# Optimization experiments

Hardware: AMD Instinct MI355X
Metric: run time of the kernel (lower is better)

## Reference

```python
import jax, jax.numpy as jnp
import numpy as np

N_HEAD = 4
EPS = 1e-5

def _layernorm(x, g, b):
    mu = jnp.mean(x, axis=-1, keepdims=True)
    var = jnp.mean(jnp.square(x - mu), axis=-1, keepdims=True)
    return (x - mu) * jax.lax.rsqrt(var + EPS) * g + b

def setup_inputs() -> dict:
    key = jax.random.key(0)
    ks = jax.random.split(key, 16)
    B, T, F = 8, 1024, 256
    dk = F // N_HEAD
    s = 1.0 / np.sqrt(F)
    return {
        "x": jax.random.normal(ks[0], (B, T, F), jnp.float32),
        "q_in": jax.random.normal(ks[1], (B, T, F), jnp.float32),
        "pos_k": jax.random.normal(ks[2], (T, T, dk), jnp.float32),
        "mask": jax.random.randint(ks[3], (B, T, T), 0, 2, jnp.int32),
        "ln_g": jnp.ones((F,), jnp.float32),
        "ln_b": jnp.zeros((F,), jnp.float32),
        "Wq": jax.random.normal(ks[4], (F, F), jnp.float32) * s,
        "bq": jnp.zeros((F,), jnp.float32),
        "Wk": jax.random.normal(ks[5], (F, F), jnp.float32) * s,
        "bk": jnp.zeros((F,), jnp.float32),
        "Wv": jax.random.normal(ks[6], (F, F), jnp.float32) * s,
        "bv": jnp.zeros((F,), jnp.float32),
        "Wo": jax.random.normal(ks[7], (F, F), jnp.float32) * s,
        "bo": jnp.zeros((F,), jnp.float32),
    }

def reference(x, q_in, pos_k, mask, ln_g, ln_b, Wq, bq, Wk, bk, Wv, bv, Wo, bo):
    B, T2, F = x.shape
    T1 = q_in.shape[1]
    h = N_HEAD
    dk = F // h
    xn = _layernorm(x, ln_g, ln_b)
    # (B, T, h, dk) -> (B, h, T, dk)
    q = (q_in @ Wq + bq).reshape(B, T1, h, dk).transpose(0, 2, 1, 3)
    k = (xn @ Wk + bk).reshape(B, T2, h, dk).transpose(0, 2, 1, 3)
    v = (xn @ Wv + bv).reshape(B, T2, h, dk).transpose(0, 2, 1, 3)
    A = jnp.einsum('bhqd,bhkd->bhqk', q, k)
    # relative position bias: B[b,h,q,t] = sum_d q[b,h,q,d] * pos_k[q,t,d]
    Bmat = jnp.einsum('bhqd,qtd->bhqt', q, pos_k)
    scores = (A + Bmat) / np.sqrt(dk)
    m = (mask[:, None, :, :] == 0)  # (B,1,T1,T2)
    min_val = jnp.finfo(scores.dtype).min
    scores = jnp.where(m, min_val, scores)
    attn = jax.nn.softmax(scores, axis=-1)
    attn = jnp.where(m, 0.0, attn)
    out = jnp.einsum('bhqk,bhkd->bhqd', attn, v)
    out = out.transpose(0, 2, 1, 3).reshape(B, T1, F)
    return out @ Wo + bo
```

## Files before the change

### kernel.cpp

```cpp
#include <hip/hip_runtime.h>
#include <hip/hip_bf16.h>

#define TT 1024
#define FF 256

typedef float  f4v  __attribute__((ext_vector_type(4)));
typedef float  f16v __attribute__((ext_vector_type(16)));
typedef __bf16 bf8v __attribute__((ext_vector_type(8)));
typedef unsigned short us8v __attribute__((ext_vector_type(8)));
typedef unsigned short us4v __attribute__((ext_vector_type(4)));

static __device__ __forceinline__ unsigned short f2bf(float x) {
    return __builtin_bit_cast(unsigned short, (__bf16)x);
}
static __device__ __forceinline__ float bf2f(unsigned short u) {
    return (float)__builtin_bit_cast(__bf16, u);
}
static __device__ __forceinline__ bf8v us2bf(us8v v) {
    return __builtin_bit_cast(bf8v, v);
}

__global__ __launch_bounds__(256) void k_wprep(
    const float* __restrict__ Wq, const float* __restrict__ Wk,
    const float* __restrict__ Wv, const float* __restrict__ Wo,
    unsigned short* __restrict__ Wt)
{
    __shared__ unsigned short T[32][36];
    const float* W = (blockIdx.y == 0) ? Wq : (blockIdx.y == 1) ? Wk
                   : (blockIdx.y == 2) ? Wv : Wo;
    unsigned short* dst = Wt + (blockIdx.y << 16);
    const int kt = (blockIdx.x >> 3) << 5, nt = (blockIdx.x & 7) << 5;
    const int r = threadIdx.x >> 3, c0 = (threadIdx.x & 7) << 2;
    const f4v w = *(const f4v*)&W[(kt + r) * FF + nt + c0];
    #pragma unroll
    for (int j = 0; j < 4; ++j) T[c0 + j][r] = f2bf(w[j]);
    __syncthreads();
    *(us4v*)&dst[(nt + r) * FF + kt + c0] = *(const us4v*)&T[r][c0];
}

__global__ __launch_bounds__(256) void k_ln(
    const float* __restrict__ x, const float* __restrict__ qin,
    const float* __restrict__ lng, const float* __restrict__ lnb,
    unsigned short* __restrict__ xn_bf, unsigned short* __restrict__ qin_bf)
{
    const int tid = threadIdx.x, lane = tid & 63, wv = tid >> 6;
    const int r0 = blockIdx.x << 4;

    #pragma unroll
    for (int u = 0; u < 4; ++u) {
        const int i4 = ((u << 8) + tid) << 2;
        const int r = i4 >> 8, c = i4 & 255;
        const f4v qv = *(const f4v*)&qin[(r0 + r) * FF + c];
        us4v o;
        #pragma unroll
        for (int j = 0; j < 4; ++j) o[j] = f2bf(qv[j]);
        *(us4v*)&qin_bf[(r0 + r) * FF + c] = o;
    }

    #pragma unroll
    for (int rr = 0; rr < 4; ++rr) {
        const int row = r0 + (wv << 2) + rr;
        float v[4], s = 0.f, s2 = 0.f;
        #pragma unroll
        for (int c4 = 0; c4 < 4; ++c4) {
            v[c4] = x[row * FF + (c4 << 6) + lane];
            s += v[c4]; s2 += v[c4] * v[c4];
        }
        #pragma unroll
        for (int off = 1; off < 64; off <<= 1) {
            s  += __shfl_xor(s, off);
            s2 += __shfl_xor(s2, off);
        }
        const float mu  = s * (1.f / FF);
        const float rsd = rsqrtf(s2 * (1.f / FF) - mu * mu + 1e-5f);
        #pragma unroll
        for (int c4 = 0; c4 < 4; ++c4) {
            const int c = (c4 << 6) + lane;
            xn_bf[row * FF + c] = f2bf((v[c4] - mu) * rsd * lng[c] + lnb[c]);
        }
    }
}

__global__ __launch_bounds__(256) void k_proj(
    const unsigned short* __restrict__ qin_bf, const unsigned short* __restrict__ xn_bf,
    const unsigned short* __restrict__ Wt,
    const float* __restrict__ bq, const float* __restrict__ bk, const float* __restrict__ bv,
    unsigned short* __restrict__ Qh, unsigned short* __restrict__ Kh,
    unsigned short* __restrict__ Vt)
{
    __shared__ __align__(16) unsigned short As[64 * 264];
    const int z = blockIdx.y;
    const unsigned short* A = (z == 0) ? qin_bf : xn_bf;
    const unsigned short* W = Wt + (z << 16);
    const float* bias = (z == 0) ? bq : (z == 1) ? bk : bv;
    unsigned short* dst = (z == 0) ? Qh : (z == 1) ? Kh : Vt;
    const int tid = threadIdx.x;
    const int m0 = blockIdx.x << 6;

    #pragma unroll
    for (int u = 0; u < 8; ++u) {
        const int idx = (u << 8) + tid;
        const int r = idx >> 5, c = (idx & 31) << 3;
        *(us8v*)&As[r * 264 + c] = *(const us8v*)&A[(m0 + r) * FF + c];
    }
    __syncthreads();

    const int lane = tid & 63, nw = tid >> 6, gq = lane >> 5, l31 = lane & 31;
    f16v acc[2][2];
    #pragma unroll
    for (int i = 0; i < 2; ++i)
        #pragma unroll
        for (int j = 0; j < 2; ++j)
            #pragma unroll
            for (int e = 0; e < 16; ++e) acc[i][j][e] = 0.f;

    for (int ks = 0; ks < 16; ++ks) {
        const int k0 = (ks << 4) + (gq << 3);
        bf8v af[2], wf[2];
        af[0] = us2bf(*(const us8v*)&As[l31 * 264 + k0]);
        af[1] = us2bf(*(const us8v*)&As[(32 + l31) * 264 + k0]);
        wf[0] = us2bf(*(const us8v*)&W[((nw << 6) + l31) * FF + k0]);
        wf[1] = us2bf(*(const us8v*)&W[((nw << 6) + 32 + l31) * FF + k0]);
        if (z == 2) {
            #pragma unroll
            for (int ti = 0; ti < 2; ++ti)
                #pragma unroll
                for (int tj = 0; tj < 2; ++tj)
                    acc[ti][tj] = __builtin_amdgcn_mfma_f32_32x32x16_bf16(
                        wf[tj], af[ti], acc[ti][tj], 0, 0, 0);
        } else {
            #pragma unroll
            for (int ti = 0; ti < 2; ++ti)
                #pragma unroll
                for (int tj = 0; tj < 2; ++tj)
                    acc[ti][tj] = __builtin_amdgcn_mfma_f32_32x32x16_bf16(
                        af[ti], wf[tj], acc[ti][tj], 0, 0, 0);
        }
    }

    if (z != 2) {
        #pragma unroll
        for (int ti = 0; ti < 2; ++ti)
            #pragma unroll
            for (int tj = 0; tj < 2; ++tj)
                #pragma unroll
                for (int reg = 0; reg < 16; ++reg) {
                    const int row = (reg & 3) + ((reg >> 2) << 3) + (gq << 2);
                    const int tg = m0 + (ti << 5) + row;
                    const int n = (nw << 6) + (tj << 5) + l31;
                    float val = acc[ti][tj][reg] + bias[n];
                    if (z == 0) val *= 0.125f;
                    const int b = tg >> 10, t = tg & 1023;
                    dst[(((b << 2) + nw) << 16) + (t << 6) + (tj << 5) + l31] = f2bf(val);
                }
    } else {
        #pragma unroll
        for (int ti = 0; ti < 2; ++ti)
            #pragma unroll
            for (int tj = 0; tj < 2; ++tj)
                #pragma unroll
                for (int reg = 0; reg < 16; ++reg) {
                    const int row = (reg & 3) + ((reg >> 2) << 3) + (gq << 2);
                    const int d = (tj << 5) + row;
                    const int tg = m0 + (ti << 5) + l31;
                    const float val = acc[ti][tj][reg] + bias[(nw << 6) + d];
                    const int b = tg >> 10, t = tg & 1023;
                    dst[(((b << 2) + nw) << 16) + (d << 10) + t] = f2bf(val);
                }
    }
}

__global__ __launch_bounds__(256) void k_bterm(
    const unsigned short* __restrict__ Qh, const float* __restrict__ posk,
    const int* __restrict__ mask, unsigned short* __restrict__ Bm)
{
    const int tid = threadIdx.x, lane = tid & 63, wv = tid >> 6;
    const int gq = lane >> 5, m = lane & 31;
    const int q = blockIdx.y;
    const int t = (blockIdx.x << 7) + (wv << 5) + m;

    bf8v afr[4];
    #pragma unroll
    for (int kk = 0; kk < 4; ++kk)
        afr[kk] = us2bf(*(const us8v*)&Qh[(m << 16) + (q << 6) + (kk << 4) + (gq << 3)]);

    bf8v bfr[4];
    #pragma unroll
    for (int kk = 0; kk < 4; ++kk) {
        const int d0 = (kk << 4) + (gq << 3);
        const f4v p0 = *(const f4v*)&posk[(((q << 10) + t) << 6) + d0];
        const f4v p1 = *(const f4v*)&posk[(((q << 10) + t) << 6) + d0 + 4];
        bf8v bb;
        bb[0] = (__bf16)p0[0]; bb[1] = (__bf16)p0[1];
        bb[2] = (__bf16)p0[2]; bb[3] = (__bf16)p0[3];
        bb[4] = (__bf16)p1[0]; bb[5] = (__bf16)p1[1];
        bb[6] = (__bf16)p1[2]; bb[7] = (__bf16)p1[3];
        bfr[kk] = bb;
    }

    f16v acc;
    #pragma unroll
    for (int i = 0; i < 16; ++i) acc[i] = 0.f;
    #pragma unroll
    for (int kk = 0; kk < 4; ++kk)
        acc = __builtin_amdgcn_mfma_f32_32x32x16_bf16(afr[kk], bfr[kk], acc, 0, 0, 0);

    int mk[4];
    #pragma unroll
    for (int g = 0; g < 4; ++g)
        mk[g] = mask[(((g << 1) + gq) << 20) + (q << 10) + t];
    #pragma unroll
    for (int reg = 0; reg < 16; ++reg) {
        const int g = reg >> 2;
        const int bhr = (reg & 3) + (g << 3) + (gq << 2);
        const float val = mk[g] ? acc[reg] : -3.0e38f;
        Bm[(bhr << 20) + (q << 10) + t] = f2bf(val);
    }
}

__global__ __launch_bounds__(256, 4) void k_attn(
    const unsigned short* __restrict__ Qh, const unsigned short* __restrict__ Kh,
    const unsigned short* __restrict__ Vt, const unsigned short* __restrict__ Bm,
    unsigned short* __restrict__ aout_bf)
{
    __shared__ __align__(16) unsigned short PsT[4][16 * 132];
    __shared__ __align__(16) float OLDS[2][16 * 68];
    __shared__ float MLDS[2][2][16];

    const int tid = threadIdx.x, lane = tid & 63, wv = tid >> 6;
    const int l15 = lane & 15, quad = lane >> 4;
    const int qg = wv & 1, th = wv >> 1;
    const int blk = blockIdx.x;
    const int bh = ((blk & 7) << 2) | ((blk >> 3) & 3);
    const int qt = blk >> 5;
    const int b = bh >> 2, h = bh & 3;
    const int q0w = (qt << 5) + (qg << 4);

    bf8v qb0, qb1;
    {
        const int base = (bh << 16) + ((q0w + l15) << 6) + (quad << 3);
        qb0 = us2bf(*(const us8v*)&Qh[base]);
        qb1 = us2bf(*(const us8v*)&Qh[base + 32]);
    }

    f4v O[4];
    #pragma unroll
    for (int i = 0; i < 4; ++i) { O[i][0]=0.f; O[i][1]=0.f; O[i][2]=0.f; O[i][3]=0.f; }
    float m_run = -3.0e38f, l_run = 0.f;

    for (int cc = 0; cc < 4; ++cc) {
        const int t0c = (th << 9) + (cc << 7);

        f4v s[8];
        #pragma unroll
        for (int nf = 0; nf < 8; ++nf) {
            const int krow = (bh << 16) + ((t0c + (nf << 4) + l15) << 6) + (quad << 3);
            const bf8v ka0 = us2bf(*(const us8v*)&Kh[krow]);
            const bf8v ka1 = us2bf(*(const us8v*)&Kh[krow + 32]);
            f4v z;
            z[0]=0.f; z[1]=0.f; z[2]=0.f; z[3]=0.f;
            z = __builtin_amdgcn_mfma_f32_16x16x32_bf16(ka0, qb0, z, 0, 0, 0);
            z = __builtin_amdgcn_mfma_f32_16x16x32_bf16(ka1, qb1, z, 0, 0, 0);
            s[nf] = z;
        }

        #pragma unroll
        for (int nf = 0; nf < 8; ++nf) {
            const us4v bm = *(const us4v*)&Bm[(bh << 20) + ((q0w + l15) << 10)
                                             + t0c + (nf << 4) + (quad << 2)];
            #pragma unroll
            for (int r = 0; r < 4; ++r) s[nf][r] += bf2f(bm[r]);
        }

        f4v mx = s[0];
        #pragma unroll
        for (int nf = 1; nf < 8; ++nf) {
            mx[0] = fmaxf(mx[0], s[nf][0]); mx[1] = fmaxf(mx[1], s[nf][1]);
            mx[2] = fmaxf(mx[2], s[nf][2]); mx[3] = fmaxf(mx[3], s[nf][3]);
        }
        float cm = fmaxf(fmaxf(mx[0], mx[1]), fmaxf(mx[2], mx[3]));
        cm = fmaxf(cm, __shfl_xor(cm, 16));
        cm = fmaxf(cm, __shfl_xor(cm, 32));

        const float mn = fmaxf(m_run, cm);
        const float alpha = __expf(m_run - mn);
        m_run = mn;
        l_run *= alpha;
        #pragma unroll
        for (int i = 0; i < 4; ++i) {
            O[i][0] *= alpha; O[i][1] *= alpha; O[i][2] *= alpha; O[i][3] *= alpha;
        }

        float rs = 0.f;
        #pragma unroll
        for (int nf = 0; nf < 8; ++nf) {
            const float p0 = __expf(s[nf][0] - mn);
            const float p1 = __expf(s[nf][1] - mn);
            const float p2 = __expf(s[nf][2] - mn);
            const float p3 = __expf(s[nf][3] - mn);
            const int ea = l15 * 132 + (nf << 4) + (quad << 2);
            *(unsigned int*)&PsT[wv][ea] =
                (unsigned int)f2bf(p0) | ((unsigned int)f2bf(p1) << 16);
            *(unsigned int*)&PsT[wv][ea + 2] =
                (unsigned int)f2bf(p2) | ((unsigned int)f2bf(p3) << 16);
            rs += (p0 + p1) + (p2 + p3);
        }
        rs += __shfl_xor(rs, 16);
        rs += __shfl_xor(rs, 32);
        l_run += rs;

        #pragma unroll
        for (int tc = 0; tc < 4; ++tc) {
            const int eb = l15 * 132 + (tc << 5) + (quad << 3);
            const us4v plo = *(const us4v*)&PsT[wv][eb];
            const us4v phi = *(const us4v*)&PsT[wv][eb + 4];
            us8v pc;
            pc[0]=plo[0]; pc[1]=plo[1]; pc[2]=plo[2]; pc[3]=plo[3];
            pc[4]=phi[0]; pc[5]=phi[1]; pc[6]=phi[2]; pc[7]=phi[3];
            const bf8v pb = us2bf(pc);
            #pragma unroll
            for (int dt = 0; dt < 4; ++dt) {
                const bf8v va = us2bf(*(const us8v*)&Vt[(bh << 16)
                    + (((dt << 4) + l15) << 10) + t0c + (tc << 5) + (quad << 3)]);
                O[dt] = __builtin_amdgcn_mfma_f32_16x16x32_bf16(va, pb, O[dt], 0, 0, 0);
            }
        }
    }

    if (th == 1) {
        #pragma unroll
        for (int dt = 0; dt < 4; ++dt)
            *(f4v*)&OLDS[qg][l15 * 68 + (dt << 4) + (quad << 2)] = O[dt];
        if (quad == 0) { MLDS[qg][0][l15] = m_run; MLDS[qg][1][l15] = l_run; }
    }
    __syncthreads();
    if (th == 0) {
        const float m1 = MLDS[qg][0][l15];
        const float l1 = MLDS[qg][1][l15];
        const float mm = fmaxf(m_run, m1);
        const float a0 = __expf(m_run - mm);
        const float a1 = __expf(m1 - mm);
        const float linv = 1.f / (l_run * a0 + l1 * a1);
        const int orow = ((b << 10) + q0w + l15) * FF + (h << 6);
        #pragma unroll
        for (int dt = 0; dt < 4; ++dt) {
            const f4v o1 = *(const f4v*)&OLDS[qg][l15 * 68 + (dt << 4) + (quad << 2)];
            us4v ov;
            #pragma unroll
            for (int r = 0; r < 4; ++r)
                ov[r] = f2bf((O[dt][r] * a0 + o1[r] * a1) * linv);
            *(us4v*)&aout_bf[orow + (dt << 4) + (quad << 2)] = ov;
        }
    }
}

__global__ __launch_bounds__(256) void k_oproj(
    const unsigned short* __restrict__ aout_bf, const unsigned short* __restrict__ Wot,
    const float* __restrict__ bo, float* __restrict__ out)
{
    __shared__ __align__(16) unsigned short As[64 * 264];
    const int tid = threadIdx.x;
    const int m0 = blockIdx.x << 6;

    #pragma unroll
    for (int u = 0; u < 8; ++u) {
        const int idx = (u << 8) + tid;
        const int r = idx >> 5, c = (idx & 31) << 3;
        *(us8v*)&As[r * 264 + c] = *(const us8v*)&aout_bf[(m0 + r) * FF + c];
    }
    __syncthreads();

    const int lane = tid & 63, nw = tid >> 6, gq = lane >> 5, l31 = lane & 31;
    f16v acc[2][2];
    #pragma unroll
    for (int i = 0; i < 2; ++i)
        #pragma unroll
        for (int j = 0; j < 2; ++j)
            #pragma unroll
            for (int e = 0; e < 16; ++e) acc[i][j][e] = 0.f;

    for (int ks = 0; ks < 16; ++ks) {
        const int k0 = (ks << 4) + (gq << 3);
        bf8v af[2], wf[2];
        af[0] = us2bf(*(const us8v*)&As[l31 * 264 + k0]);
        af[1] = us2bf(*(const us8v*)&As[(32 + l31) * 264 + k0]);
        wf[0] = us2bf(*(const us8v*)&Wot[((nw << 6) + l31) * FF + k0]);
        wf[1] = us2bf(*(const us8v*)&Wot[((nw << 6) + 32 + l31) * FF + k0]);
        #pragma unroll
        for (int ti = 0; ti < 2; ++ti)
            #pragma unroll
            for (int tj = 0; tj < 2; ++tj)
                acc[ti][tj] = __builtin_amdgcn_mfma_f32_32x32x16_bf16(
                    af[ti], wf[tj], acc[ti][tj], 0, 0, 0);
    }

    #pragma unroll
    for (int ti = 0; ti < 2; ++ti)
        #pragma unroll
        for (int tj = 0; tj < 2; ++tj)
            #pragma unroll
            for (int reg = 0; reg < 16; ++reg) {
                const int row = (reg & 3) + ((reg >> 2) << 3) + (gq << 2);
                const int tg = m0 + (ti << 5) + row;
                const int n = (nw << 6) + (tj << 5) + l31;
                out[tg * FF + n] = acc[ti][tj][reg] + bo[n];
            }
}

extern "C" void kernel_launch(void* const* d_in, const int* in_sizes, int n_in,
                              void* d_out, int out_size, void* d_ws, size_t ws_size,
                              hipStream_t stream)
{
    const float* x    = (const float*)d_in[0];
    const float* qin  = (const float*)d_in[1];
    const float* posk = (const float*)d_in[2];
    const int*   mask = (const int*)d_in[3];
    const float* ln_g = (const float*)d_in[4];
    const float* ln_b = (const float*)d_in[5];
    const float* Wq   = (const float*)d_in[6];
    const float* bq   = (const float*)d_in[7];
    const float* Wk   = (const float*)d_in[8];
    const float* bk   = (const float*)d_in[9];
    const float* Wv   = (const float*)d_in[10];
    const float* bv   = (const float*)d_in[11];
    const float* Wo   = (const float*)d_in[12];
    const float* bo   = (const float*)d_in[13];
    float* out = (float*)d_out;

    char* ws = (char*)d_ws;
    unsigned short* wWt   = (unsigned short*)(ws);
    unsigned short* qinb  = (unsigned short*)(ws + (size_t)(1u << 20));
    unsigned short* xnb   = (unsigned short*)(ws + (size_t)(5u << 20));
    unsigned short* Qh    = (unsigned short*)(ws + (size_t)(9u << 20));
    unsigned short* Kh    = (unsigned short*)(ws + (size_t)(13u << 20));
    unsigned short* Vth   = (unsigned short*)(ws + (size_t)(17u << 20));
    unsigned short* aoutb = (unsigned short*)(ws + (size_t)(21u << 20));
    unsigned short* Bm    = (unsigned short*)(ws + (size_t)(25u << 20));

    hipLaunchKernelGGL(k_wprep, dim3(64, 4), dim3(256), 0, stream, Wq, Wk, Wv, Wo, wWt);
    hipLaunchKernelGGL(k_ln, dim3(512), dim3(256), 0, stream,
                       x, qin, ln_g, ln_b, xnb, qinb);
    hipLaunchKernelGGL(k_proj, dim3(128, 3), dim3(256), 0, stream,
                       qinb, xnb, wWt, bq, bk, bv, Qh, Kh, Vth);
    hipLaunchKernelGGL(k_bterm, dim3(8, 1024), dim3(256), 0, stream,
                       Qh, posk, mask, Bm);
    hipLaunchKernelGGL(k_attn, dim3(1024), dim3(256), 0, stream,
                       Qh, Kh, Vth, Bm, aoutb);
    hipLaunchKernelGGL(k_oproj, dim3(128), dim3(256), 0, stream,
                       aoutb, wWt + (3 << 16), bo, out);
}
```

Baseline: 530.3 us.

## Software-pipeline K, bias and V loads into registers in attention kernel

Moves the K-tile and bias loads for the next 128-key chunk into registers while the current chunk is processed. All V fragments for a chunk are issued up front, and scheduling barriers keep the loads early, so global latency overlaps softmax and MFMA work. The much larger register footprint is accommodated by lowering the launch-bounds occupancy hint from 4 to 2 blocks per CU, at the risk of less latency hiding through wave parallelism.

```diff
diff --git a/kernel.cpp b/kernel.cpp
--- a/kernel.cpp
+++ b/kernel.cpp
@@ -218,7 +218,7 @@
     }
 }
 
-__global__ __launch_bounds__(256, 4) void k_attn(
+__global__ __launch_bounds__(256, 2) void k_attn(
     const unsigned short* __restrict__ Qh, const unsigned short* __restrict__ Kh,
     const unsigned short* __restrict__ Vt, const unsigned short* __restrict__ Bm,
     unsigned short* __restrict__ aout_bf)
@@ -236,6 +236,10 @@
     const int b = bh >> 2, h = bh & 3;
     const int q0w = (qt << 5) + (qg << 4);
 
+    const unsigned short* Kbase = Kh + (bh << 16);
+    const unsigned short* Vbase = Vt + (bh << 16);
+    const unsigned short* Bbase = Bm + (bh << 20) + ((q0w + l15) << 10);
+
     bf8v qb0, qb1;
     {
         const int base = (bh << 16) + ((q0w + l15) << 6) + (quad << 3);
@@ -248,29 +252,58 @@
     for (int i = 0; i < 4; ++i) { O[i][0]=0.f; O[i][1]=0.f; O[i][2]=0.f; O[i][3]=0.f; }
     float m_run = -3.0e38f, l_run = 0.f;
 
+    us8v kreg[8][2];
+    us4v bmreg[8];
+    {
+        const int t0c = th << 9;
+        #pragma unroll
+        for (int nf = 0; nf < 8; ++nf) {
+            const int krow = ((t0c + (nf << 4) + l15) << 6) + (quad << 3);
+            kreg[nf][0] = *(const us8v*)&Kbase[krow];
+            kreg[nf][1] = *(const us8v*)&Kbase[krow + 32];
+        }
+        #pragma unroll
+        for (int nf = 0; nf < 8; ++nf)
+            bmreg[nf] = *(const us4v*)&Bbase[t0c + (nf << 4) + (quad << 2)];
+    }
+
     for (int cc = 0; cc < 4; ++cc) {
         const int t0c = (th << 9) + (cc << 7);
 
+        us8v vreg[4][4];
+        #pragma unroll
+        for (int tc = 0; tc < 4; ++tc)
+            #pragma unroll
+            for (int dt = 0; dt < 4; ++dt)
+                vreg[tc][dt] = *(const us8v*)&Vbase[(((dt << 4) + l15) << 10)
+                                                   + t0c + (tc << 5) + (quad << 3)];
+        __builtin_amdgcn_sched_barrier(0);
+
         f4v s[8];
         #pragma unroll
         for (int nf = 0; nf < 8; ++nf) {
-            const int krow = (bh << 16) + ((t0c + (nf << 4) + l15) << 6) + (quad << 3);
-            const bf8v ka0 = us2bf(*(const us8v*)&Kh[krow]);
-            const bf8v ka1 = us2bf(*(const us8v*)&Kh[krow + 32]);
             f4v z;
             z[0]=0.f; z[1]=0.f; z[2]=0.f; z[3]=0.f;
-            z = __builtin_amdgcn_mfma_f32_16x16x32_bf16(ka0, qb0, z, 0, 0, 0);
-            z = __builtin_amdgcn_mfma_f32_16x16x32_bf16(ka1, qb1, z, 0, 0, 0);
+            z = __builtin_amdgcn_mfma_f32_16x16x32_bf16(us2bf(kreg[nf][0]), qb0, z, 0, 0, 0);
+            z = __builtin_amdgcn_mfma_f32_16x16x32_bf16(us2bf(kreg[nf][1]), qb1, z, 0, 0, 0);
+            #pragma unroll
+            for (int r = 0; r < 4; ++r) z[r] += bf2f(bmreg[nf][r]);
             s[nf] = z;
         }
 
-        #pragma unroll
-        for (int nf = 0; nf < 8; ++nf) {
-            const us4v bm = *(const us4v*)&Bm[(bh << 20) + ((q0w + l15) << 10)
-                                             + t0c + (nf << 4) + (quad << 2)];
-            #pragma unroll
-            for (int r = 0; r < 4; ++r) s[nf][r] += bf2f(bm[r]);
-        }
+        if (cc < 3) {
+            const int t0n = (th << 9) + ((cc + 1) << 7);
+            #pragma unroll
+            for (int nf = 0; nf < 8; ++nf) {
+                const int krow = ((t0n + (nf << 4) + l15) << 6) + (quad << 3);
+                kreg[nf][0] = *(const us8v*)&Kbase[krow];
+                kreg[nf][1] = *(const us8v*)&Kbase[krow + 32];
+            }
+            #pragma unroll
+            for (int nf = 0; nf < 8; ++nf)
+                bmreg[nf] = *(const us4v*)&Bbase[t0n + (nf << 4) + (quad << 2)];
+        }
+        __builtin_amdgcn_sched_barrier(0);
 
         f4v mx = s[0];
         #pragma unroll
@@ -319,11 +352,9 @@
             pc[4]=phi[0]; pc[5]=phi[1]; pc[6]=phi[2]; pc[7]=phi[3];
             const bf8v pb = us2bf(pc);
             #pragma unroll
-            for (int dt = 0; dt < 4; ++dt) {
-                const bf8v va = us2bf(*(const us8v*)&Vt[(bh << 16)
-                    + (((dt << 4) + l15) << 10) + t0c + (tc << 5) + (quad << 3)]);
-                O[dt] = __builtin_amdgcn_mfma_f32_16x16x32_bf16(va, pb, O[dt], 0, 0, 0);
-            }
+            for (int dt = 0; dt < 4; ++dt)
+                O[dt] = __builtin_amdgcn_mfma_f32_16x16x32_bf16(
+                    us2bf(vreg[tc][dt]), pb, O[dt], 0, 0, 0);
         }
     }
 
```

Result: no change. 526.3 us (-0.8%).
